# Optimization experiments

Hardware: AMD Instinct MI355X
Metric: run time of the kernel (lower is better)

Reference implementation:

```python
import jax, jax.numpy as jnp
import numpy as np

DIM = 1024
HEADS = 16
HEAD_DIM = DIM // HEADS
SCALE = HEAD_DIM ** -0.5


def setup_inputs() -> dict:
    key = jax.random.key(0)
    k1, k2, k3, k4, k5, k6 = jax.random.split(key, 6)
    B, N = 2, 2048
    x = jax.random.normal(k1, (B, N, DIM), dtype=jnp.float32)
    importance_weights = jax.random.uniform(k2, (B, N), dtype=jnp.float32)
    # torch nn.Linear(dim, 3*dim, bias=False): weight [3*dim, dim]; store transposed for x @ W
    W_qkv = jax.random.normal(k3, (DIM, 3 * DIM), dtype=jnp.float32) * (DIM ** -0.5)
    W_proj = jax.random.normal(k4, (DIM, DIM), dtype=jnp.float32) * (DIM ** -0.5)
    b_proj = jax.random.normal(k5, (DIM,), dtype=jnp.float32) * 0.01
    persistence_bias = jnp.zeros((1, HEADS, 1, 1), dtype=jnp.float32)
    return {"x": x, "importance_weights": importance_weights, "W_qkv": W_qkv,
            "W_proj": W_proj, "b_proj": b_proj, "persistence_bias": persistence_bias}


def reference(x, importance_weights, W_qkv, W_proj, b_proj, persistence_bias):
    B, N, C = x.shape
    qkv = (x @ W_qkv).reshape(B, N, 3, HEADS, HEAD_DIM)
    qkv = jnp.transpose(qkv, (2, 0, 3, 1, 4))  # [3, B, H, N, hd]
    q, k, v = qkv[0], qkv[1], qkv[2]
    attn = jnp.einsum('bhqd,bhkd->bhqk', q, k) * SCALE  # [B,H,N,N]
    # importance: [B,N] -> [B,1,N,1], broadcasts over heads and key dim
    attn = attn + persistence_bias + importance_weights[:, None, :, None] * 0.1
    attn = jax.nn.softmax(attn, axis=-1)
    out = jnp.einsum('bhqk,bhkd->bhqd', attn, v)  # [B,H,N,hd]
    out = jnp.transpose(out, (0, 2, 1, 3)).reshape(B, N, C)
    return out @ W_proj + b_proj
```

## Files before the change

### kernel.cpp

```cpp
#include <hip/hip_runtime.h>
#include <hip/hip_bf16.h>
#include <cstdint>
#include <cstddef>


typedef __attribute__((ext_vector_type(8))) short short8;
typedef __attribute__((ext_vector_type(4))) float f32x4;
typedef __attribute__((ext_vector_type(16))) float f32x16;

__device__ __forceinline__ short f2bf(float f) {
    union { float f; uint32_t u; } v; v.f = f;
    uint32_t r = (v.u + 0x7fffu + ((v.u >> 16) & 1u)) >> 16;
    return (short)r;
}

__device__ __forceinline__ uint32_t cvtpk(float lo, float hi) {
    uint32_t r;
    asm("v_cvt_pk_bf16_f32 %0, %1, %2" : "=v"(r) : "v"(lo), "v"(hi));
    return r;
}

__device__ __forceinline__ float fexp2(float x) {
#if __has_builtin(__builtin_amdgcn_exp2f)
    return __builtin_amdgcn_exp2f(x);
#else
    return exp2f(x);
#endif
}

__device__ __forceinline__ void plswap(uint32_t& a, uint32_t& b) {
#if __has_builtin(__builtin_amdgcn_permlane32_swap)
    auto r = __builtin_amdgcn_permlane32_swap((int)a, (int)b, false, false);
    a = (uint32_t)r[0]; b = (uint32_t)r[1];
#else
    int lane = threadIdx.x & 63;
    uint32_t sa = (uint32_t)__shfl_xor((int)a, 32), sb = (uint32_t)__shfl_xor((int)b, 32);
    uint32_t na = (lane < 32) ? a : sb, nb = (lane < 32) ? sa : b;
    a = na; b = nb;
#endif
}

#define GLOAD_LDS16(g, l)                                                          \
    __builtin_amdgcn_global_load_lds(                                              \
        (const __attribute__((address_space(1))) unsigned int*)(g),                \
        (__attribute__((address_space(3))) unsigned int*)(l), 16, 0, 0)

__global__ __launch_bounds__(256) void bda_f32_to_bf16(const float* __restrict__ in,
                                                       short* __restrict__ out, int n8) {
    int i = blockIdx.x * 256 + threadIdx.x;
    if (i >= n8) return;
    const float* p = in + (size_t)i * 8;
    short8 r;
#pragma unroll
    for (int j = 0; j < 8; ++j) r[j] = f2bf(p[j]);
    *(short8*)(out + (size_t)i * 8) = r;
}

__global__ __launch_bounds__(256) void bda_transpose_w(const float* __restrict__ W,
                                                       short* __restrict__ Wt,
                                                       int K, int Nc) {
    __shared__ float tile[32][33];
    int n0 = blockIdx.x * 32, k0 = blockIdx.y * 32;
    int tx = threadIdx.x, ty = threadIdx.y;
#pragma unroll
    for (int i = 0; i < 32; i += 8)
        tile[ty + i][tx] = W[(size_t)(k0 + ty + i) * Nc + n0 + tx];
    __syncthreads();
#pragma unroll
    for (int i = 0; i < 32; i += 8)
        Wt[(size_t)(n0 + ty + i) * K + k0 + tx] = f2bf(tile[tx][ty + i]);
}

template <int EPI, int BN>
__global__ __launch_bounds__(256) void bda_gemm_bt(
    const short* __restrict__ A, const short* __restrict__ Bt,
    int Ncols, int K,
    short* __restrict__ Qd, short* __restrict__ Kd, short* __restrict__ Vtd,
    float* __restrict__ Cout, const float* __restrict__ bias)
{
    constexpr int NF = BN / 32;
    __shared__ short As[128 * 32];
    __shared__ short Bs[BN * 32];
    __shared__ short Tv[(EPI == 1) ? 64 * 136 : 4];

    const int tid = threadIdx.x;
    const int wid = tid >> 6, lane = tid & 63;
    const int lr = lane & 15, lk = lane >> 4;
    const int nbc = Ncols / BN;
    const int brow = blockIdx.x / nbc, bcol = blockIdx.x % nbc;
    const int wr = wid >> 1, wc = wid & 1;

    const f32x4 zero = {0.f, 0.f, 0.f, 0.f};
    f32x4 acc[4][NF];
#pragma unroll
    for (int m = 0; m < 4; ++m)
#pragma unroll
        for (int n = 0; n < NF; ++n) acc[m][n] = zero;

    const short* aSrc = A  + (size_t)(brow * 128 + (tid >> 2)) * K + (tid & 3) * 8;
    const short* bSrc = Bt + (size_t)(bcol * BN + (tid >> 2)) * K + (tid & 3) * 8;
    char* ldsA = (char*)As + wid * 1024;
    char* ldsB = (char*)Bs + wid * 1024;
    const size_t rowskip = (size_t)64 * K;

    for (int k0 = 0; k0 < K; k0 += 32) {
        GLOAD_LDS16(aSrc + k0, ldsA);
        GLOAD_LDS16(aSrc + rowskip + k0, ldsA + 4096);
        GLOAD_LDS16(bSrc + k0, ldsB);
        if constexpr (BN == 128) GLOAD_LDS16(bSrc + rowskip + k0, ldsB + 4096);
        __syncthreads();

        short8 aF[4], bF[NF];
#pragma unroll
        for (int m = 0; m < 4; ++m)
            aF[m] = *(const short8*)(As + (wr * 64 + m * 16 + lr) * 32 + lk * 8);
#pragma unroll
        for (int n = 0; n < NF; ++n)
            bF[n] = *(const short8*)(Bs + (wc * (BN / 2) + n * 16 + lr) * 32 + lk * 8);
#pragma unroll
        for (int m = 0; m < 4; ++m)
#pragma unroll
            for (int n = 0; n < NF; ++n)
                acc[m][n] = __builtin_amdgcn_mfma_f32_16x16x32_bf16(aF[m], bF[n], acc[m][n], 0, 0, 0);
        __syncthreads();
    }

    if constexpr (EPI == 1) {
        if (bcol < 16) {
            const float QSCALE = 0.125f * 1.44269504088896340736f;
#pragma unroll
            for (int n = 0; n < 4; ++n) {
                int c = bcol * 128 + wc * 64 + n * 16 + lr;
                int s = c >> 10, r = c & 1023;
                int h = r >> 6, d = r & 63;
#pragma unroll
                for (int m = 0; m < 4; ++m)
#pragma unroll
                    for (int j = 0; j < 4; ++j) {
                        int mg = brow * 128 + wr * 64 + m * 16 + lk * 4 + j;
                        int b = mg >> 11, nn = mg & 2047;
                        size_t bh = (size_t)(b * 16 + h);
                        float v = acc[m][n][j];
                        if (s == 0) Qd[(bh * 2048 + nn) * 64 + d] = f2bf(v * QSCALE);
                        else        Kd[(bh * 2048 + nn) * 64 + d] = f2bf(v);
                    }
            }
        } else {
            const int h0 = (bcol - 16) * 2;
            const int bb = brow >> 4;
            const int nn0 = (brow & 15) * 128;
#pragma unroll
            for (int hb = 0; hb < 2; ++hb) {
                if (wc == hb) {
#pragma unroll
                    for (int n = 0; n < 4; ++n) {
                        int d = n * 16 + lr;
#pragma unroll
                        for (int m = 0; m < 4; ++m) {
                            int nn = wr * 64 + m * 16 + lk * 4;
                            *(uint32_t*)&Tv[d * 136 + nn]     = cvtpk(acc[m][n][0], acc[m][n][1]);
                            *(uint32_t*)&Tv[d * 136 + nn + 2] = cvtpk(acc[m][n][2], acc[m][n][3]);
                        }
                    }
                }
                __syncthreads();
                size_t bh = (size_t)(bb * 16 + h0 + hb);
#pragma unroll
                for (int it = 0; it < 4; ++it) {
                    int cidx = it * 256 + tid;
                    int d = cidx >> 4, c16 = cidx & 15;
                    short8 v = *(const short8*)(&Tv[d * 136 + c16 * 8]);
                    *(short8*)(Vtd + (bh * 64 + d) * 2048 + nn0 + c16 * 8) = v;
                }
                if (hb == 0) __syncthreads();
            }
        }
    } else {
#pragma unroll
        for (int n = 0; n < NF; ++n) {
            int c = bcol * BN + wc * (BN / 2) + n * 16 + lr;
            float bv = bias[c];
#pragma unroll
            for (int m = 0; m < 4; ++m)
#pragma unroll
                for (int j = 0; j < 4; ++j) {
                    int mg = brow * 128 + wr * 64 + m * 16 + lk * 4 + j;
                    Cout[(size_t)mg * Ncols + c] = acc[m][n][j] + bv;
                }
        }
    }
}

__global__ __launch_bounds__(256, 2) void bda_attn3(const short* __restrict__ Q,
                                                    const short* __restrict__ K,
                                                    const short* __restrict__ Vt,
                                                    short* __restrict__ O)
{
    __shared__ char Kbuf[2][16384];
    __shared__ char Vbuf[2][16384];

    const int tid = threadIdx.x;
    const int wid = tid >> 6, lane = tid & 63;
    const int lq = lane & 31, hi = lane >> 5;

    const int bid = blockIdx.x;
    const int L = (bid & 7) * 64 + (bid >> 3);
    const int bh = L >> 4, qc = L & 15;
    const int b = bh >> 4, h = bh & 15;

    const short* Qg = Q  + (size_t)bh * 2048 * 64;
    const short* Kg = K  + (size_t)bh * 2048 * 64;
    const short* Vg = Vt + (size_t)bh * 64 * 2048;
    const int q0 = qc * 128 + wid * 32;

    short8 qf[4];
#pragma unroll
    for (int dk = 0; dk < 4; ++dk)
        qf[dk] = *(const short8*)(Qg + (size_t)(q0 + lq) * 64 + dk * 16 + hi * 8);

    const f32x16 z16 = {};
    f32x16 accO0 = z16, accO1 = z16;
    float lsum = 0.f;

    const int kRow0 = wid * 8 + (lane >> 3);
    const int kSwz  = ((lane & 7) ^ ((lane >> 3) & 7)) * 8;
    const int vRow0 = wid * 4 + (lane >> 4);
    const int vSwz  = ((lane & 15) ^ vRow0) * 8;

    auto STAGE = [&](int bufi, int kvb) {
#pragma unroll
        for (int g = 0; g < 4; ++g) {
            GLOAD_LDS16(Kg + (size_t)(kvb + g * 32 + kRow0) * 64 + kSwz,
                        Kbuf[bufi] + g * 4096 + wid * 1024);
            GLOAD_LDS16(Vg + (size_t)(g * 16 + vRow0) * 2048 + kvb + vSwz,
                        Vbuf[bufi] + g * 4096 + wid * 1024);
        }
    };

    STAGE(0, 0);
    int cur = 0;

    for (int t = 0; t < 16; ++t) {
        __syncthreads();
        if (t < 15) STAGE(cur ^ 1, (t + 1) * 128);

        const char* Kl = Kbuf[cur];
        const char* Vl = Vbuf[cur];

        f32x16 ps[4];
#pragma unroll
        for (int qd = 0; qd < 4; ++qd) ps[qd] = z16;
        __builtin_amdgcn_s_setprio(1);
#pragma unroll
        for (int dk = 0; dk < 4; ++dk) {
#pragma unroll
            for (int qd = 0; qd < 4; ++qd) {
                int row = qd * 32 + lq;
                short8 kf = *(const short8*)(Kl + row * 128 + (((dk * 2 + hi) ^ (lq & 7)) << 4));
                ps[qd] = __builtin_amdgcn_mfma_f32_32x32x16_bf16(kf, qf[dk], ps[qd], 0, 0, 0);
            }
        }
        __builtin_amdgcn_s_setprio(0);

#pragma unroll
        for (int qd = 0; qd < 4; ++qd)
#pragma unroll
            for (int r = 0; r < 16; ++r) ps[qd][r] = fexp2(ps[qd][r]);

        f32x16 sv = (ps[0] + ps[1]) + (ps[2] + ps[3]);
        float t0 = (sv[0] + sv[1]) + (sv[2] + sv[3]);
        float t1 = (sv[4] + sv[5]) + (sv[6] + sv[7]);
        float t2 = (sv[8] + sv[9]) + (sv[10] + sv[11]);
        float t3 = (sv[12] + sv[13]) + (sv[14] + sv[15]);
        float ts = (t0 + t1) + (t2 + t3);
        ts += __shfl_xor(ts, 32);
        lsum += ts;

        __builtin_amdgcn_s_setprio(1);
#pragma unroll
        for (int SC = 0; SC < 8; ++SC) {
            const f32x16& PF = ps[SC >> 1];
            const int o = (SC & 1) * 8;
            uint32_t w0 = cvtpk(PF[o + 0], PF[o + 1]), w1 = cvtpk(PF[o + 2], PF[o + 3]);
            uint32_t w2 = cvtpk(PF[o + 4], PF[o + 5]), w3 = cvtpk(PF[o + 6], PF[o + 7]);
            plswap(w0, w2);
            plswap(w1, w3);
            union { uint32_t w[4]; short8 v; } pw;
            pw.w[0] = w0; pw.w[1] = w1; pw.w[2] = w2; pw.w[3] = w3;
            const int vs = ((SC * 2 + hi) ^ (lq & 15)) << 4;
            short8 v0 = *(const short8*)(Vl + lq * 256 + vs);
            short8 v1 = *(const short8*)(Vl + (32 + lq) * 256 + vs);
            accO0 = __builtin_amdgcn_mfma_f32_32x32x16_bf16(v0, pw.v, accO0, 0, 0, 0);
            accO1 = __builtin_amdgcn_mfma_f32_32x32x16_bf16(v1, pw.v, accO1, 0, 0, 0);
        }
        __builtin_amdgcn_s_setprio(0);
        cur ^= 1;
    }

    float inv = 1.0f / lsum;
    char* trW = &Kbuf[0][0] + wid * 4096;
    const int sw = (lq & 7) << 4;
#pragma unroll
    for (int r = 0; r < 16; r += 2) {
        int d0 = (r & 3) + 8 * (r >> 2) + 4 * hi;
        *(uint32_t*)(trW + lq * 128 + ((d0 * 2) ^ sw))      = cvtpk(accO0[r] * inv, accO0[r + 1] * inv);
        *(uint32_t*)(trW + lq * 128 + ((64 + d0 * 2) ^ sw)) = cvtpk(accO1[r] * inv, accO1[r + 1] * inv);
    }
#pragma unroll
    for (int c2 = 0; c2 < 4; ++c2) {
        int qr = c2 * 8 + (lane >> 3);
        short8 v = *(const short8*)(trW + qr * 128 + ((((lane & 7) << 4)) ^ ((qr & 7) << 4)));
        *(short8*)(O + (size_t)(b * 2048 + q0 + qr) * 1024 + h * 64 + (lane & 7) * 8) = v;
    }
}

extern "C" void kernel_launch(void* const* d_in, const int* in_sizes, int n_in,
                              void* d_out, int out_size, void* d_ws, size_t ws_size,
                              hipStream_t stream) {
    const float* x      = (const float*)d_in[0];
    const float* Wqkv   = (const float*)d_in[2];
    const float* Wproj  = (const float*)d_in[3];
    const float* bproj  = (const float*)d_in[4];
    float* out = (float*)d_out;

    char* ws = (char*)d_ws;
    const size_t MB = (size_t)1 << 20;
    short* xb     = (short*)(ws + 0 * MB);
    short* Wqkvt  = (short*)(ws + 8 * MB);
    short* Wprojt = (short*)(ws + 14 * MB);
    short* Qws    = (short*)(ws + 16 * MB);
    short* Kws    = (short*)(ws + 24 * MB);
    short* Vtws   = (short*)(ws + 32 * MB);
    short* Ows    = (short*)(ws + 40 * MB);

    bda_f32_to_bf16<<<2048, 256, 0, stream>>>(x, xb, 524288);
    bda_transpose_w<<<dim3(96, 32), dim3(32, 8), 0, stream>>>(Wqkv, Wqkvt, 1024, 3072);
    bda_transpose_w<<<dim3(32, 32), dim3(32, 8), 0, stream>>>(Wproj, Wprojt, 1024, 1024);

    bda_gemm_bt<1, 128><<<32 * 24, 256, 0, stream>>>(xb, Wqkvt, 3072, 1024,
                                                     Qws, Kws, Vtws, nullptr, nullptr);
    bda_attn3<<<512, 256, 0, stream>>>(Qws, Kws, Vtws, Ows);

    bda_gemm_bt<2, 64><<<32 * 16, 256, 0, stream>>>(Ows, Wprojt, 1024, 1024,
                                                    nullptr, nullptr, nullptr, out, bproj);
}
```

Before: 190.8 us.

## Split attention KV range in two halves with a separate combine kernel

```diff
diff --git a/kernel.cpp b/kernel.cpp
--- a/kernel.cpp
+++ b/kernel.cpp
@@ -17,6 +17,12 @@
 __device__ __forceinline__ uint32_t cvtpk(float lo, float hi) {
     uint32_t r;
     asm("v_cvt_pk_bf16_f32 %0, %1, %2" : "=v"(r) : "v"(lo), "v"(hi));
+    return r;
+}
+
+__device__ __forceinline__ uint32_t pkrtz(float lo, float hi) {
+    uint32_t r;
+    asm("v_cvt_pkrtz_f16_f32 %0, %1, %2" : "=v"(r) : "v"(lo), "v"(hi));
     return r;
 }
 
@@ -87,7 +93,9 @@
     const int wid = tid >> 6, lane = tid & 63;
     const int lr = lane & 15, lk = lane >> 4;
     const int nbc = Ncols / BN;
-    const int brow = blockIdx.x / nbc, bcol = blockIdx.x % nbc;
+    const int nwg = gridDim.x;
+    const int bidx = (blockIdx.x & 7) * (nwg >> 3) + (blockIdx.x >> 3);
+    const int brow = bidx / nbc, bcol = bidx % nbc;
     const int wr = wid >> 1, wc = wid & 1;
 
     const f32x4 zero = {0.f, 0.f, 0.f, 0.f};
@@ -188,6 +196,168 @@
                     Cout[(size_t)mg * Ncols + c] = acc[m][n][j] + bv;
                 }
         }
+    }
+}
+
+__global__ __launch_bounds__(256, 4) void bda_attn4(const short* __restrict__ Q,
+                                                    const short* __restrict__ K,
+                                                    const short* __restrict__ Vt,
+                                                    uint32_t* __restrict__ OTp,
+                                                    float* __restrict__ Lp)
+{
+    __shared__ char Kbuf[2][8192];
+    __shared__ char Vbuf[2][8192];
+
+    const int tid = threadIdx.x;
+    const int wid = tid >> 6, lane = tid & 63;
+    const int lq = lane & 31, hi = lane >> 5;
+
+    const int bid = blockIdx.x;
+    const int L = (bid & 7) * 128 + (bid >> 3);
+    const int bh = L >> 5, qc = (L >> 1) & 15, kvh = L & 1;
+
+    const short* Qg = Q  + (size_t)bh * 2048 * 64;
+    const short* Kg = K  + (size_t)bh * 2048 * 64 + (size_t)kvh * 1024 * 64;
+    const short* Vg = Vt + (size_t)bh * 64 * 2048 + kvh * 1024;
+    const int q0 = qc * 128 + wid * 32;
+
+    short8 qf[4];
+#pragma unroll
+    for (int dk = 0; dk < 4; ++dk)
+        qf[dk] = *(const short8*)(Qg + (size_t)(q0 + lq) * 64 + dk * 16 + hi * 8);
+
+    const f32x16 z16 = {};
+    f32x16 accO0 = z16, accO1 = z16;
+    float lsum = 0.f;
+
+    const int sRow = wid * 8 + (lane >> 3);
+    const int sSwz = ((lane & 7) ^ (lane >> 3)) * 8;
+
+    auto STAGE = [&](int bufi, int kvb) {
+#pragma unroll
+        for (int g = 0; g < 2; ++g) {
+            GLOAD_LDS16(Kg + (size_t)(kvb + g * 32 + sRow) * 64 + sSwz,
+                        Kbuf[bufi] + g * 4096 + wid * 1024);
+            GLOAD_LDS16(Vg + (size_t)(g * 32 + sRow) * 2048 + kvb + sSwz,
+                        Vbuf[bufi] + g * 4096 + wid * 1024);
+        }
+    };
+
+    STAGE(0, 0);
+    int cur = 0;
+
+    for (int t = 0; t < 16; ++t) {
+        __syncthreads();
+        if (t < 15) STAGE(cur ^ 1, (t + 1) * 64);
+
+        const char* Kl = Kbuf[cur];
+        const char* Vl = Vbuf[cur];
+
+        f32x16 ps[2];
+        ps[0] = z16; ps[1] = z16;
+        __builtin_amdgcn_s_setprio(1);
+#pragma unroll
+        for (int dk = 0; dk < 4; ++dk) {
+#pragma unroll
+            for (int qd = 0; qd < 2; ++qd) {
+                short8 kf = *(const short8*)(Kl + (qd * 32 + lq) * 128 +
+                                             (((dk * 2 + hi) ^ (lq & 7)) << 4));
+                ps[qd] = __builtin_amdgcn_mfma_f32_32x32x16_bf16(kf, qf[dk], ps[qd], 0, 0, 0);
+            }
+        }
+        __builtin_amdgcn_s_setprio(0);
+
+#pragma unroll
+        for (int qd = 0; qd < 2; ++qd)
+#pragma unroll
+            for (int r = 0; r < 16; ++r) ps[qd][r] = fexp2(ps[qd][r]);
+
+        f32x16 sv = ps[0] + ps[1];
+        float t0 = (sv[0] + sv[1]) + (sv[2] + sv[3]);
+        float t1 = (sv[4] + sv[5]) + (sv[6] + sv[7]);
+        float t2 = (sv[8] + sv[9]) + (sv[10] + sv[11]);
+        float t3 = (sv[12] + sv[13]) + (sv[14] + sv[15]);
+        float ts = (t0 + t1) + (t2 + t3);
+        ts += __shfl_xor(ts, 32);
+        lsum += ts;
+
+        __builtin_amdgcn_s_setprio(1);
+#pragma unroll
+        for (int SC = 0; SC < 4; ++SC) {
+            const f32x16& PF = ps[SC >> 1];
+            const int o = (SC & 1) * 8;
+            uint32_t w0 = cvtpk(PF[o + 0], PF[o + 1]), w1 = cvtpk(PF[o + 2], PF[o + 3]);
+            uint32_t w2 = cvtpk(PF[o + 4], PF[o + 5]), w3 = cvtpk(PF[o + 6], PF[o + 7]);
+            plswap(w0, w2);
+            plswap(w1, w3);
+            union { uint32_t w[4]; short8 v; } pw;
+            pw.w[0] = w0; pw.w[1] = w1; pw.w[2] = w2; pw.w[3] = w3;
+            const int vs = ((SC * 2 + hi) ^ (lq & 7)) << 4;
+            short8 v0 = *(const short8*)(Vl + lq * 128 + vs);
+            short8 v1 = *(const short8*)(Vl + (32 + lq) * 128 + vs);
+            accO0 = __builtin_amdgcn_mfma_f32_32x32x16_bf16(v0, pw.v, accO0, 0, 0, 0);
+            accO1 = __builtin_amdgcn_mfma_f32_32x32x16_bf16(v1, pw.v, accO1, 0, 0, 0);
+        }
+        __builtin_amdgcn_s_setprio(0);
+        cur ^= 1;
+    }
+
+    float inv = 1.0f / lsum;
+    uint32_t* base = OTp + (size_t)((kvh * 32 + bh) * 32) * 2048 + q0 + lq;
+#pragma unroll
+    for (int r = 0; r < 16; r += 2) {
+        int dp = ((r & 3) >> 1) + 4 * (r >> 2) + 2 * hi;
+        base[(size_t)dp * 2048]        = pkrtz(accO0[r] * inv, accO0[r + 1] * inv);
+        base[(size_t)(dp + 16) * 2048] = pkrtz(accO1[r] * inv, accO1[r + 1] * inv);
+    }
+    if (hi == 0) Lp[(size_t)(kvh * 32 + bh) * 2048 + q0 + lq] = lsum;
+}
+
+__global__ __launch_bounds__(256) void bda_combine(const uint32_t* __restrict__ OTp,
+                                                   const float* __restrict__ Lp,
+                                                   short* __restrict__ Ows)
+{
+    __shared__ float T[128][65];
+    __shared__ float W1[128], W2[128];
+    const int tid = threadIdx.x;
+    const int bh = blockIdx.x >> 4, qb = blockIdx.x & 15;
+    const int b = bh >> 4, h = bh & 15;
+    const int q0 = qb * 128;
+
+    const uint32_t* O1 = OTp + (size_t)bh * 32 * 2048;
+    const uint32_t* O2 = OTp + (size_t)(32 + bh) * 32 * 2048;
+
+    if (tid < 128) {
+        float l1 = Lp[(size_t)bh * 2048 + q0 + tid];
+        float l2 = Lp[(size_t)(32 + bh) * 2048 + q0 + tid];
+        float inv = 1.0f / (l1 + l2);
+        W1[tid] = l1 * inv; W2[tid] = l2 * inv;
+    }
+    __syncthreads();
+
+    union H2 { uint32_t u; _Float16 h[2]; };
+#pragma unroll
+    for (int it = 0; it < 16; ++it) {
+        int idx = it * 256 + tid;
+        int dp = idx >> 7, q = idx & 127;
+        H2 a, c;
+        a.u = O1[(size_t)dp * 2048 + q0 + q];
+        c.u = O2[(size_t)dp * 2048 + q0 + q];
+        float w1 = W1[q], w2 = W2[q];
+        T[q][dp * 2]     = (float)a.h[0] * w1 + (float)c.h[0] * w2;
+        T[q][dp * 2 + 1] = (float)a.h[1] * w1 + (float)c.h[1] * w2;
+    }
+    __syncthreads();
+#pragma unroll
+    for (int it = 0; it < 4; ++it) {
+        int q = it * 32 + (tid >> 3), d0 = (tid & 7) * 8;
+        short8 o;
+#pragma unroll
+        for (int j = 0; j < 8; j += 2) {
+            uint32_t w = cvtpk(T[q][d0 + j], T[q][d0 + j + 1]);
+            o[j] = (short)(w & 0xffff); o[j + 1] = (short)(w >> 16);
+        }
+        *(short8*)(Ows + (size_t)(b * 2048 + q0 + q) * 1024 + h * 64 + d0) = o;
     }
 }
 
@@ -332,6 +502,8 @@
     short* Kws    = (short*)(ws + 24 * MB);
     short* Vtws   = (short*)(ws + 32 * MB);
     short* Ows    = (short*)(ws + 40 * MB);
+    uint32_t* OTp = (uint32_t*)(ws + 48 * MB);
+    float* Lp     = (float*)(ws + 64 * MB);
 
     bda_f32_to_bf16<<<2048, 256, 0, stream>>>(x, xb, 524288);
     bda_transpose_w<<<dim3(96, 32), dim3(32, 8), 0, stream>>>(Wqkv, Wqkvt, 1024, 3072);
@@ -339,7 +511,13 @@
 
     bda_gemm_bt<1, 128><<<32 * 24, 256, 0, stream>>>(xb, Wqkvt, 3072, 1024,
                                                      Qws, Kws, Vtws, nullptr, nullptr);
-    bda_attn3<<<512, 256, 0, stream>>>(Qws, Kws, Vtws, Ows);
+
+    if (ws_size >= 65 * MB) {
+        bda_attn4<<<1024, 256, 0, stream>>>(Qws, Kws, Vtws, OTp, Lp);
+        bda_combine<<<512, 256, 0, stream>>>(OTp, Lp, Ows);
+    } else {
+        bda_attn3<<<512, 256, 0, stream>>>(Qws, Kws, Vtws, Ows);
+    }
 
     bda_gemm_bt<2, 64><<<32 * 16, 256, 0, stream>>>(Ows, Wprojt, 1024, 1024,
                                                     nullptr, nullptr, nullptr, out, bproj);
```

Result: slower. 198.0 us (+3.8%).
